# Kernel optimization log

Hardware: AMD Instinct MI355X
Metric: run time of the kernel (lower is better)

## Reference

```python
import jax, jax.numpy as jnp
import numpy as np

DIM = 1024
N_HEADS = 16
HEAD_DIM = DIM // N_HEADS
HIDDEN = 2816
SEQ = 4096
BATCH = 1
NORM_EPS = 1e-5


def setup_inputs() -> dict:
    key = jax.random.key(0)
    ks = jax.random.split(key, 9)
    s = 1.0 / np.sqrt(DIM)
    return {
        "x": jax.random.normal(ks[0], (BATCH, SEQ, DIM), jnp.float32),
        "wq": jax.random.normal(ks[1], (DIM, DIM), jnp.float32) * s,
        "wk": jax.random.normal(ks[2], (DIM, DIM), jnp.float32) * s,
        "wv": jax.random.normal(ks[3], (DIM, DIM), jnp.float32) * s,
        "wo": jax.random.normal(ks[4], (DIM, DIM), jnp.float32) * s,
        "w1": jax.random.normal(ks[5], (DIM, HIDDEN), jnp.float32) * s,
        "w2": jax.random.normal(ks[6], (HIDDEN, DIM), jnp.float32) / np.sqrt(HIDDEN),
        "w3": jax.random.normal(ks[7], (DIM, HIDDEN), jnp.float32) * s,
        "g_attn_norm": jnp.ones((DIM,), jnp.float32),
        "g_ffn_norm": jnp.ones((DIM,), jnp.float32),
    }


def rmsnorm(x, g):
    # x: [b, s, d]; compute in fp32 as in the torch module, then cast back
    xf = x.astype(jnp.float32)
    n = xf * jax.lax.rsqrt(jnp.mean(xf * xf, axis=-1, keepdims=True) + NORM_EPS)
    return n.astype(x.dtype) * g


def attention(x, wq, wk, wv, wo):
    b, s, _ = x.shape
    q = (x @ wq).reshape(b, s, N_HEADS, HEAD_DIM).transpose(0, 2, 1, 3)  # [b,h,s,hd]
    k = (x @ wk).reshape(b, s, N_HEADS, HEAD_DIM).transpose(0, 2, 1, 3)
    v = (x @ wv).reshape(b, s, N_HEADS, HEAD_DIM).transpose(0, 2, 1, 3)
    scores = jnp.einsum("bhqd,bhkd->bhqk", q, k) / np.sqrt(HEAD_DIM)
    causal = jnp.tril(jnp.ones((s, s), bool))
    scores = jnp.where(causal, scores, -jnp.inf)
    probs = jax.nn.softmax(scores.astype(jnp.float32), axis=-1).astype(q.dtype)
    out = jnp.einsum("bhqk,bhkd->bhqd", probs, v)
    out = out.transpose(0, 2, 1, 3).reshape(b, s, DIM)
    return out @ wo


def feed_forward(x, w1, w2, w3):
    return (jax.nn.silu(x @ w1) * (x @ w3)) @ w2


def reference(x, wq, wk, wv, wo, w1, w2, w3, g_attn_norm, g_ffn_norm):
    h = x + attention(rmsnorm(x, g_attn_norm), wq, wk, wv, wo)
    out = h + feed_forward(rmsnorm(h, g_ffn_norm), w1, w2, w3)
    return out
```

## Files before the change

### kernel.cpp

```cpp
#include <hip/hip_runtime.h>
#include <stdint.h>


typedef unsigned short u16;
typedef unsigned int u32;
typedef __attribute__((ext_vector_type(8))) short short8;
typedef __attribute__((ext_vector_type(4))) float f32x4;

#define GLD16(G, L) __builtin_amdgcn_global_load_lds( \
    (__attribute__((address_space(1))) void*)(G),      \
    (__attribute__((address_space(3))) void*)(L), 16, 0, 0)

__device__ __forceinline__ u16 f2bf(float f) {
  u32 u = __builtin_bit_cast(u32, f);
  u32 r = u + 0x7fffu + ((u >> 16) & 1u);
  return (u16)(r >> 16);
}
__device__ __forceinline__ float bf2f(u16 b) {
  u32 u = (u32)b << 16;
  return __builtin_bit_cast(float, u);
}
__device__ __forceinline__ u32 pk_bf16(float lo, float hi) {
  u32 r;
  asm("v_cvt_pk_bf16_f32 %0, %1, %2" : "=v"(r) : "v"(lo), "v"(hi));
  return r;
}

__global__ __launch_bounds__(256) void k_prep(const float* __restrict__ wq,
                                              const float* __restrict__ wk,
                                              const float* __restrict__ wv,
                                              const float* __restrict__ wo,
                                              const float* __restrict__ w1,
                                              const float* __restrict__ w3,
                                              const float* __restrict__ w2f,
                                              u16* __restrict__ wqkvo_t,
                                              u16* __restrict__ w13_t,
                                              u16* __restrict__ w2_t) {
  const int bid = blockIdx.x;
  const float* in;
  u16* o;
  int R, C, c0, r0;
  if (bid < 4096) {
    const int z = bid >> 10, r = bid & 1023;
    in = (z == 0) ? wq : (z == 1) ? wk : (z == 2) ? wv : wo;
    o = wqkvo_t + (size_t)z * 1024 * 1024;
    R = 1024; C = 1024;
    c0 = (r & 31) * 32; r0 = (r >> 5) * 32;
  } else if (bid < 9728) {
    int r = bid - 4096;
    const int z = r / 2816; r %= 2816;
    in = z ? w3 : w1;
    o = w13_t + (size_t)z * 2816 * 1024;
    R = 1024; C = 2816;
    c0 = (r % 88) * 32; r0 = (r / 88) * 32;
  } else {
    const int r = bid - 9728;
    in = w2f; o = w2_t;
    R = 2816; C = 1024;
    c0 = (r & 31) * 32; r0 = (r >> 5) * 32;
  }
  __shared__ float t[32][33];
  const int tx = threadIdx.x & 31, ty = threadIdx.x >> 5;
#pragma unroll
  for (int i = 0; i < 32; i += 8)
    t[ty + i][tx] = in[(size_t)(r0 + ty + i) * C + (c0 + tx)];
  __syncthreads();
#pragma unroll
  for (int i = 0; i < 32; i += 8)
    o[(size_t)(c0 + ty + i) * R + (r0 + tx)] = f2bf(t[tx][ty + i]);
}

__global__ __launch_bounds__(256) void k_rms(const float* __restrict__ x,
                                             const float* __restrict__ g,
                                             u16* __restrict__ o) {
  const int row = blockIdx.x, tid = threadIdx.x;
  const float4 v = ((const float4*)(x + (size_t)row * 1024))[tid];
  float ss = v.x * v.x + v.y * v.y + v.z * v.z + v.w * v.w;
#pragma unroll
  for (int ofs = 32; ofs > 0; ofs >>= 1) ss += __shfl_xor(ss, ofs);
  __shared__ float red[4];
  if ((tid & 63) == 0) red[tid >> 6] = ss;
  __syncthreads();
  const float s = rsqrtf((red[0] + red[1] + red[2] + red[3]) * (1.f / 1024.f) + 1e-5f);
  const float4 gv = ((const float4*)g)[tid];
  u32 lo = (u32)f2bf(v.x * s * gv.x) | ((u32)f2bf(v.y * s * gv.y) << 16);
  u32 hi = (u32)f2bf(v.z * s * gv.z) | ((u32)f2bf(v.w * s * gv.w) << 16);
  *(uint2*)(o + (size_t)row * 1024 + tid * 4) = make_uint2(lo, hi);
}

template <int EPI, int TN>
__global__ __launch_bounds__(256) void k_gemm(const u16* __restrict__ A,
                                              const u16* __restrict__ Bt,
                                              u16* __restrict__ Obf,
                                              float* __restrict__ Of,
                                              const float* __restrict__ Rz,
                                              int M, int N, int K) {
  constexpr int NFR = TN / 32;
  __shared__ __align__(16) u16 As[2][128 * 32];
  __shared__ __align__(16) u16 Bs[2][TN * 32];
  const int tid = threadIdx.x;
  const int lane = tid & 63, wave = tid >> 6;
  const int wr = wave >> 1, wc = wave & 1;
  const int li = lane & 15, lg = lane >> 4;
  const int row0 = blockIdx.y * 128, col0 = blockIdx.x * TN;

  f32x4 acc[4][NFR] = {};
  const int sr = tid >> 2, sc = (tid & 3) * 8;
  const u16* ag = A + (size_t)(row0 + sr) * K + sc;
  const u16* bg = Bt + (size_t)(col0 + sr) * K + sc;
  const size_t rstep = (size_t)64 * K;

  GLD16(ag, &As[0][tid * 8]);
  GLD16(ag + rstep, &As[0][tid * 8 + 2048]);
  GLD16(bg, &Bs[0][tid * 8]);
  if constexpr (TN == 128) GLD16(bg + rstep, &Bs[0][tid * 8 + 2048]);
  __syncthreads();

  int cur = 0;
  for (int k0 = 0; k0 < K; k0 += 32) {
    const int nxt = cur ^ 1;
    if (k0 + 32 < K) {
      GLD16(ag + k0 + 32, &As[nxt][tid * 8]);
      GLD16(ag + rstep + k0 + 32, &As[nxt][tid * 8 + 2048]);
      GLD16(bg + k0 + 32, &Bs[nxt][tid * 8]);
      if constexpr (TN == 128) GLD16(bg + rstep + k0 + 32, &Bs[nxt][tid * 8 + 2048]);
    }
    short8 af[4], bfr[NFR];
#pragma unroll
    for (int m = 0; m < 4; ++m)
      af[m] = *(const short8*)(&As[cur][(wr * 64 + m * 16 + li) * 32 + lg * 8]);
#pragma unroll
    for (int n = 0; n < NFR; ++n)
      bfr[n] = *(const short8*)(&Bs[cur][(wc * (TN / 2) + n * 16 + li) * 32 + lg * 8]);
#pragma unroll
    for (int m = 0; m < 4; ++m)
#pragma unroll
      for (int n = 0; n < NFR; ++n)
        acc[m][n] = __builtin_amdgcn_mfma_f32_16x16x32_bf16(af[m], bfr[n], acc[m][n], 0, 0, 0);
    __syncthreads();
    cur = nxt;
  }

#pragma unroll
  for (int m = 0; m < 4; ++m) {
    const int row = row0 + wr * 64 + m * 16 + lg * 4;
#pragma unroll
    for (int n = 0; n < NFR; ++n) {
      const int col = col0 + wc * (TN / 2) + n * 16 + li;
#pragma unroll
      for (int r = 0; r < 4; ++r) {
        const size_t idx = (size_t)(row + r) * N + col;
        if (EPI == 0) Obf[idx] = f2bf(acc[m][n][r]);
        else          Of[idx] = acc[m][n][r] + Rz[idx];
      }
    }
  }
}

__global__ __launch_bounds__(256) void k_ffn13(const u16* __restrict__ A,
                                               const u16* __restrict__ B1,
                                               const u16* __restrict__ B3,
                                               u16* __restrict__ O,
                                               int M, int N, int K) {
  __shared__ __align__(16) u16 As[2][128 * 32];
  __shared__ __align__(16) u16 B1s[2][64 * 32];
  __shared__ __align__(16) u16 B3s[2][64 * 32];
  const int tid = threadIdx.x;
  const int lane = tid & 63, wave = tid >> 6;
  const int wr = wave >> 1, wc = wave & 1;
  const int li = lane & 15, lg = lane >> 4;
  const int row0 = blockIdx.y * 128, col0 = blockIdx.x * 64;

  f32x4 a1[4][2] = {}, a3[4][2] = {};
  const int sr = tid >> 2, sc = (tid & 3) * 8;
  const u16* ag = A + (size_t)(row0 + sr) * K + sc;
  const u16* b1g = B1 + (size_t)(col0 + sr) * K + sc;
  const u16* b3g = B3 + (size_t)(col0 + sr) * K + sc;
  const size_t rstep = (size_t)64 * K;

  GLD16(ag, &As[0][tid * 8]);
  GLD16(ag + rstep, &As[0][tid * 8 + 2048]);
  GLD16(b1g, &B1s[0][tid * 8]);
  GLD16(b3g, &B3s[0][tid * 8]);
  __syncthreads();

  int cur = 0;
  for (int k0 = 0; k0 < K; k0 += 32) {
    const int nxt = cur ^ 1;
    if (k0 + 32 < K) {
      GLD16(ag + k0 + 32, &As[nxt][tid * 8]);
      GLD16(ag + rstep + k0 + 32, &As[nxt][tid * 8 + 2048]);
      GLD16(b1g + k0 + 32, &B1s[nxt][tid * 8]);
      GLD16(b3g + k0 + 32, &B3s[nxt][tid * 8]);
    }
    short8 af[4], b1f[2], b3f[2];
#pragma unroll
    for (int m = 0; m < 4; ++m)
      af[m] = *(const short8*)(&As[cur][(wr * 64 + m * 16 + li) * 32 + lg * 8]);
#pragma unroll
    for (int n = 0; n < 2; ++n) {
      b1f[n] = *(const short8*)(&B1s[cur][(wc * 32 + n * 16 + li) * 32 + lg * 8]);
      b3f[n] = *(const short8*)(&B3s[cur][(wc * 32 + n * 16 + li) * 32 + lg * 8]);
    }
#pragma unroll
    for (int m = 0; m < 4; ++m)
#pragma unroll
      for (int n = 0; n < 2; ++n) {
        a1[m][n] = __builtin_amdgcn_mfma_f32_16x16x32_bf16(af[m], b1f[n], a1[m][n], 0, 0, 0);
        a3[m][n] = __builtin_amdgcn_mfma_f32_16x16x32_bf16(af[m], b3f[n], a3[m][n], 0, 0, 0);
      }
    __syncthreads();
    cur = nxt;
  }

#pragma unroll
  for (int m = 0; m < 4; ++m) {
    const int row = row0 + wr * 64 + m * 16 + lg * 4;
#pragma unroll
    for (int n = 0; n < 2; ++n) {
      const int col = col0 + wc * 32 + n * 16 + li;
#pragma unroll
      for (int r = 0; r < 4; ++r) {
        const float g1 = a1[m][n][r], g3 = a3[m][n][r];
        const float sl = g1 / (1.f + __expf(-g1));
        O[(size_t)(row + r) * N + col] = f2bf(sl * g3);
      }
    }
  }
}

__global__ __launch_bounds__(512) void k_attn(const u16* __restrict__ qkv,
                                              u16* __restrict__ Opart,
                                              float* __restrict__ ml) {
  const int LD = 3072;
  const int bid = blockIdx.x;
  const int qb = 31 - (bid >> 5);
  const int h = (bid >> 1) & 15;
  const int j = bid & 1;
  const int tid = threadIdx.x, lane = tid & 63, w = tid >> 6;
  const int li = lane & 15, lg = lane >> 4;
  const int swzB = (li & 7) << 4;
  const float QS = 0.125f * 1.44269504f;
  const float FM = 12.0f;

  __shared__ __align__(16) u16 Ks[64 * 64];
  __shared__ __align__(16) u16 Vt[64 * 64];
  __shared__ __align__(16) u16 Ps[8 * 16 * 64];

  const int krow = tid >> 3;
  const u16* kg = qkv + 1024 + h * 64 + ((tid & 7) ^ (krow & 7)) * 8;
  u16* klds = Ks + tid * 8;

  const int vd0 = (tid & 31) * 2;
  const int vkq = tid >> 5;
  const u16* vg = qkv + 2048 + h * 64 + vd0;
  u16* vl0 = Vt + (size_t)vd0 * 64 + (((vkq * 8) ^ ((vd0 & 7) << 4)) >> 1);
  u16* vl1 = Vt + (size_t)(vd0 + 1) * 64 + (((vkq * 8) ^ (((vd0 + 1) & 7) << 4)) >> 1);
  u16* pw = Ps + w * 1024 + li * 64;

  const int q0 = qb * 128;
  const int t0 = j ? (qb + 1) : 0;
  const int t1 = j ? (2 * qb + 2) : (qb + 1);
  const int qrow = q0 + w * 16 + li;
  const int wqmax = q0 + w * 16 + 15;

  const u16* qp = qkv + (size_t)qrow * LD + h * 64;
  short8 qf0, qf1;
#pragma unroll
  for (int jj = 0; jj < 8; ++jj) {
    qf0[jj] = (short)f2bf(bf2f(qp[lg * 8 + jj]) * QS);
    qf1[jj] = (short)f2bf(bf2f(qp[32 + lg * 8 + jj]) * QS);
  }

  float lsm = 0.f;
  f32x4 accO[4] = {};
  uint4 kld;
  u32 vld[4];
  kld = *(const uint4*)(kg + (size_t)(t0 * 64 + krow) * LD);
#pragma unroll
  for (int i = 0; i < 4; ++i)
    vld[i] = *(const u32*)(vg + (size_t)(t0 * 64 + vkq * 4 + i) * LD);

  for (int t = t0; t < t1; ++t) {
    const int k0 = t * 64;
    __syncthreads();
    *(uint4*)klds = kld;
    {
      u32 lo0 = (vld[0] & 0xffffu) | (vld[1] << 16);
      u32 lo1 = (vld[2] & 0xffffu) | (vld[3] << 16);
      u32 hi0 = (vld[0] >> 16) | (vld[1] & 0xffff0000u);
      u32 hi1 = (vld[2] >> 16) | (vld[3] & 0xffff0000u);
      *(uint2*)vl0 = make_uint2(lo0, lo1);
      *(uint2*)vl1 = make_uint2(hi0, hi1);
    }
    __syncthreads();
    if (t + 1 < t1) {
      kld = *(const uint4*)(kg + (size_t)((t + 1) * 64 + krow) * LD);
      const u16* vp = vg + (size_t)(t + 1) * 64 * LD;
#pragma unroll
      for (int i = 0; i < 4; ++i) vld[i] = *(const u32*)(vp + (size_t)(vkq * 4 + i) * LD);
    }

    if (k0 <= wqmax) {
      f32x4 st[4];
#pragma unroll
      for (int f = 0; f < 4; ++f) {
        const u16* kp = Ks + (size_t)(f * 16 + li) * 64;
        const short8 ka0 = *(const short8*)(kp + (((lg * 16) ^ swzB) >> 1));
        const short8 ka1 = *(const short8*)(kp + (((64 + lg * 16) ^ swzB) >> 1));
        f32x4 z = {-FM, -FM, -FM, -FM};
        z = __builtin_amdgcn_mfma_f32_16x16x32_bf16(ka0, qf0, z, 0, 0, 0);
        st[f] = __builtin_amdgcn_mfma_f32_16x16x32_bf16(ka1, qf1, z, 0, 0, 0);
      }
      if (!(k0 + 63 <= q0 + w * 16)) {
#pragma unroll
        for (int f = 0; f < 4; ++f)
#pragma unroll
          for (int r = 0; r < 4; ++r) {
            const int kg2 = k0 + f * 16 + lg * 4 + r;
            if (kg2 > qrow) st[f][r] = -1e30f;
          }
      }
      float psum = 0.f;
#pragma unroll
      for (int f = 0; f < 4; ++f) {
        const float p0 = __builtin_amdgcn_exp2f(st[f][0]);
        const float p1 = __builtin_amdgcn_exp2f(st[f][1]);
        const float p2 = __builtin_amdgcn_exp2f(st[f][2]);
        const float p3 = __builtin_amdgcn_exp2f(st[f][3]);
        psum += (p0 + p1) + (p2 + p3);
        *(uint2*)(pw + (((f * 32 + lg * 8) ^ swzB) >> 1)) =
            make_uint2(pk_bf16(p0, p1), pk_bf16(p2, p3));
      }
      psum += __shfl_xor(psum, 16);
      psum += __shfl_xor(psum, 32);
      lsm += psum;

#pragma unroll
      for (int kk = 0; kk < 2; ++kk) {
        const int cofs = ((kk * 64 + lg * 16) ^ swzB) >> 1;
        const short8 pf = *(const short8*)(pw + cofs);
#pragma unroll
        for (int n = 0; n < 4; ++n) {
          const short8 vf = *(const short8*)(Vt + (size_t)(n * 16 + li) * 64 + cofs);
          accO[n] = __builtin_amdgcn_mfma_f32_16x16x32_bf16(vf, pf, accO[n], 0, 0, 0);
        }
      }
    }
  }

  const int item = (h * 32 + qb) * 2 + j;
  u16* op = Opart + (size_t)item * 8192 + (w * 16 + li) * 64 + lg * 4;
#pragma unroll
  for (int n = 0; n < 4; ++n)
    *(uint2*)(op + n * 16) = make_uint2(pk_bf16(accO[n][0], accO[n][1]),
                                        pk_bf16(accO[n][2], accO[n][3]));
  if (lg == 0) ml[item * 128 + w * 16 + li] = lsm;
}

__global__ __launch_bounds__(256) void k_amerge(const u16* __restrict__ Opart,
                                                const float* __restrict__ ml,
                                                u16* __restrict__ o) {
  const int b = blockIdx.x;
  const int h = b & 15, qb = b >> 4;
  const int q = threadIdx.x >> 1;
  const int dh = (threadIdx.x & 1) * 32;
  const int i0 = (h * 32 + qb) * 2;
  const float l0 = ml[i0 * 128 + q];
  const float l1 = ml[(i0 + 1) * 128 + q];
  const float r = 1.f / (l0 + l1);
  const u16* p0 = Opart + (size_t)i0 * 8192 + q * 64 + dh;
  const u16* p1 = p0 + 8192;
  u16* op = o + (size_t)(qb * 128 + q) * 1024 + h * 64 + dh;
#pragma unroll
  for (int dd = 0; dd < 32; dd += 4) {
    const uint2 a = *(const uint2*)(p0 + dd);
    const uint2 c = *(const uint2*)(p1 + dd);
    const float s0 = bf2f((u16)a.x) + bf2f((u16)c.x);
    const float s1 = bf2f((u16)(a.x >> 16)) + bf2f((u16)(c.x >> 16));
    const float s2 = bf2f((u16)a.y) + bf2f((u16)c.y);
    const float s3 = bf2f((u16)(a.y >> 16)) + bf2f((u16)(c.y >> 16));
    *(uint2*)(op + dd) = make_uint2(pk_bf16(s0 * r, s1 * r), pk_bf16(s2 * r, s3 * r));
  }
}

extern "C" void kernel_launch(void* const* d_in, const int* in_sizes, int n_in,
                              void* d_out, int out_size, void* d_ws, size_t ws_size,
                              hipStream_t stream) {
  const float* x  = (const float*)d_in[0];
  const float* wq = (const float*)d_in[1];
  const float* wk = (const float*)d_in[2];
  const float* wv = (const float*)d_in[3];
  const float* wo = (const float*)d_in[4];
  const float* w1 = (const float*)d_in[5];
  const float* w2 = (const float*)d_in[6];
  const float* w3 = (const float*)d_in[7];
  const float* ga = (const float*)d_in[8];
  const float* gf = (const float*)d_in[9];
  float* out = (float*)d_out;

  char* p = (char*)d_ws;
  auto take = [&](size_t n) { char* r = p; p += (n + 255) & ~(size_t)255; return r; };
  u16* wqkvo_t = (u16*)take(4ull * 1024 * 1024 * 2);
  u16* w13_t   = (u16*)take(2ull * 2816 * 1024 * 2);
  u16* w2_t    = (u16*)take(1024ull * 2816 * 2);
  u16* xn      = (u16*)take(4096ull * 1024 * 2);
  u16* qkvb    = (u16*)take(4096ull * 3072 * 2);
  u16* atn     = (u16*)take(4096ull * 1024 * 2);
  char* uni    = take(48234496);
  u16* Opart   = (u16*)uni;
  float* mlb   = (float*)(uni + 1024ull * 8192 * 2);
  float* hb    = (float*)uni;
  u16* hn      = (u16*)(uni + 4096ull * 1024 * 4);
  u16* ffb     = (u16*)(uni + 4096ull * 1024 * 6);

  u16* wqkv_t = wqkvo_t;
  u16* wo_t   = wqkvo_t + 3ull * 1024 * 1024;
  u16* w1_t   = w13_t;
  u16* w3_t   = w13_t + 2816ull * 1024;

  k_prep<<<12544, 256, 0, stream>>>(wq, wk, wv, wo, w1, w3, w2, wqkvo_t, w13_t, w2_t);

  k_rms<<<4096, 256, 0, stream>>>(x, ga, xn);
  k_gemm<0, 128><<<dim3(24, 32), 256, 0, stream>>>(xn, wqkv_t, qkvb, nullptr, nullptr, 4096, 3072, 1024);
  k_attn<<<1024, 512, 0, stream>>>(qkvb, Opart, mlb);
  k_amerge<<<512, 256, 0, stream>>>(Opart, mlb, atn);
  k_gemm<1, 64><<<dim3(16, 32), 256, 0, stream>>>(atn, wo_t, nullptr, hb, x, 4096, 1024, 1024);
  k_rms<<<4096, 256, 0, stream>>>(hb, gf, hn);
  k_ffn13<<<dim3(44, 32), 256, 0, stream>>>(hn, w1_t, w3_t, ffb, 4096, 2816, 1024);
  k_gemm<1, 64><<<dim3(16, 32), 256, 0, stream>>>(ffb, w2_t, nullptr, out, hb, 4096, 1024, 2816);
}
```

Before: 260.3 us.

## Triple-buffer FFN gate/up GEMM with explicit vmcnt waits

Converts the fused w1/w3 GEMM kernel from double to triple buffering in LDS, prefetching two K-steps ahead. Each iteration waits only on the older batch of loads with a partial s_waitcnt vmcnt instead of a full __syncthreads. The aim is to hide global-to-LDS load latency behind the MFMAs. LDS use per block rises by half, which may reduce occupancy, and the hand-written waitcnt bookkeeping is fragile.

Result: no change. 261.5 us (+0.4%).

```diff
diff --git a/kernel.cpp b/kernel.cpp
--- a/kernel.cpp
+++ b/kernel.cpp
@@ -162,9 +162,9 @@
                                                const u16* __restrict__ B3,
                                                u16* __restrict__ O,
                                                int M, int N, int K) {
-  __shared__ __align__(16) u16 As[2][128 * 32];
-  __shared__ __align__(16) u16 B1s[2][64 * 32];
-  __shared__ __align__(16) u16 B3s[2][64 * 32];
+  __shared__ __align__(16) u16 As[3][128 * 32];
+  __shared__ __align__(16) u16 B1s[3][64 * 32];
+  __shared__ __align__(16) u16 B3s[3][64 * 32];
   const int tid = threadIdx.x;
   const int lane = tid & 63, wave = tid >> 6;
   const int wr = wave >> 1, wc = wave & 1;
@@ -177,22 +177,25 @@
   const u16* b1g = B1 + (size_t)(col0 + sr) * K + sc;
   const u16* b3g = B3 + (size_t)(col0 + sr) * K + sc;
   const size_t rstep = (size_t)64 * K;
-
-  GLD16(ag, &As[0][tid * 8]);
-  GLD16(ag + rstep, &As[0][tid * 8 + 2048]);
-  GLD16(b1g, &B1s[0][tid * 8]);
-  GLD16(b3g, &B3s[0][tid * 8]);
-  __syncthreads();
-
-  int cur = 0;
-  for (int k0 = 0; k0 < K; k0 += 32) {
-    const int nxt = cur ^ 1;
-    if (k0 + 32 < K) {
-      GLD16(ag + k0 + 32, &As[nxt][tid * 8]);
-      GLD16(ag + rstep + k0 + 32, &As[nxt][tid * 8 + 2048]);
-      GLD16(b1g + k0 + 32, &B1s[nxt][tid * 8]);
-      GLD16(b3g + k0 + 32, &B3s[nxt][tid * 8]);
-    }
+  const int NS = K >> 5;
+
+  auto issue = [&](int k, int buf) {
+    GLD16(ag + k * 32, &As[buf][tid * 8]);
+    GLD16(ag + rstep + k * 32, &As[buf][tid * 8 + 2048]);
+    GLD16(b1g + k * 32, &B1s[buf][tid * 8]);
+    GLD16(b3g + k * 32, &B3s[buf][tid * 8]);
+  };
+
+  issue(0, 0);
+  issue(1, 1);
+  asm volatile("s_waitcnt vmcnt(4)" ::: "memory");
+  __builtin_amdgcn_s_barrier();
+  __builtin_amdgcn_sched_barrier(0);
+
+  for (int k = 0; k < NS; ++k) {
+    const int cur = k % 3;
+    if (k + 2 < NS) issue(k + 2, (k + 2) % 3);
+
     short8 af[4], b1f[2], b3f[2];
 #pragma unroll
     for (int m = 0; m < 4; ++m)
@@ -209,8 +212,13 @@
         a1[m][n] = __builtin_amdgcn_mfma_f32_16x16x32_bf16(af[m], b1f[n], a1[m][n], 0, 0, 0);
         a3[m][n] = __builtin_amdgcn_mfma_f32_16x16x32_bf16(af[m], b3f[n], a3[m][n], 0, 0, 0);
       }
-    __syncthreads();
-    cur = nxt;
+
+    if (k + 1 < NS) {
+      if (k + 2 < NS) asm volatile("s_waitcnt vmcnt(4)" ::: "memory");
+      else            asm volatile("s_waitcnt vmcnt(0)" ::: "memory");
+      __builtin_amdgcn_s_barrier();
+      __builtin_amdgcn_sched_barrier(0);
+    }
   }
 
 #pragma unroll
```
